# Performance work log

Measured on AMD Instinct MI355X. Metric: run time of the kernel, lower is better.

The kernel has to match this reference:

```python
import jax, jax.numpy as jnp
import numpy as np

DIM = 768
NUM_HEADS = 8
HEAD_DIM = DIM // NUM_HEADS


def setup_inputs() -> dict:
    key = jax.random.key(0)
    k1, k2, k3, k4, k5 = jax.random.split(key, 5)
    B, C, H, W = 16, DIM, 32, 32
    x = jax.random.normal(k1, (B, C, H, W), dtype=jnp.float32)
    # Conv2d 1x1 weights expressed as [out_ch, in_ch] matrices
    w_qkv = jax.random.normal(k2, (3 * C, C), dtype=jnp.float32) * (C ** -0.5)
    b_qkv = jax.random.normal(k3, (3 * C,), dtype=jnp.float32) * 0.02
    w_proj = jax.random.normal(k4, (C, C), dtype=jnp.float32) * (C ** -0.5)
    b_proj = jax.random.normal(k5, (C,), dtype=jnp.float32) * 0.02
    return {"x": x, "w_qkv": w_qkv, "b_qkv": b_qkv, "w_proj": w_proj, "b_proj": b_proj}


def reference(x, w_qkv, b_qkv, w_proj, b_proj):
    B, C, H, W = x.shape
    N = H * W
    nh, hd = NUM_HEADS, C // NUM_HEADS
    xf = x.astype(jnp.float32).reshape(B, C, N)  # bcn
    # 1x1 conv == channel matmul
    qkv = jnp.einsum('oc,bcn->bon', w_qkv, xf) + b_qkv[None, :, None]
    qkv = qkv.reshape(B, 3, nh, hd, N)
    q, k, v = qkv[:, 0], qkv[:, 1], qkv[:, 2]  # [B, nh, hd, N]
    s = hd ** -0.25  # scale split between q and k as in the original
    attn = jnp.einsum('bhdn,bhdm->bhnm', q * s, k * s)  # [B, nh, N, N]
    attn = attn - jax.lax.stop_gradient(jnp.max(attn, axis=-1, keepdims=True))
    attn = jnp.clip(attn, -88.0, 88.0)
    attn = jax.nn.softmax(attn, axis=-1)
    # dropout is identity in eval mode
    out = jnp.einsum('bhnm,bhdm->bhdn', attn, v)  # [B, nh, hd, N]
    out = out.reshape(B, C, N)
    out = jnp.einsum('oc,bcn->bon', w_proj, out) + b_proj[None, :, None]
    return out.reshape(B, C, H, W).astype(x.dtype)
```

## Files before the change

kernel.cpp:

```cpp
#include <hip/hip_runtime.h>
#include <stdint.h>

typedef __attribute__((ext_vector_type(4))) float f32x4;
typedef __attribute__((ext_vector_type(16))) float f32x16;
typedef __attribute__((ext_vector_type(8))) short bf16x8;

#define SQKV 0.38372606f

__device__ __forceinline__ unsigned short f2bf(float f) {
  union { float f; unsigned u; } v; v.f = f;
  unsigned r = v.u + 0x7FFFu + ((v.u >> 16) & 1u);
  return (unsigned short)(r >> 16);
}

__device__ __forceinline__ unsigned cvt_pk_bf16(float a, float b) {
  unsigned r;
  asm volatile("v_cvt_pk_bf16_f32 %0, %1, %2" : "=v"(r) : "v"(a), "v"(b));
  return r;
}
__device__ __forceinline__ void permswap(unsigned &a, unsigned &b) {
  asm volatile("v_permlane32_swap_b32 %0, %1" : "+v"(a), "+v"(b));
}

__device__ __forceinline__ void glds16(const unsigned short* g, unsigned short* l) {
  __builtin_amdgcn_global_load_lds(
      (const __attribute__((address_space(1))) void*)g,
      (__attribute__((address_space(3))) void*)l, 16, 0, 0);
}

__global__ __launch_bounds__(256) void k_convert(const float* __restrict__ src,
                                                 unsigned short* __restrict__ dst,
                                                 int n4) {
  int i = blockIdx.x * 256 + threadIdx.x;
  if (i >= n4) return;
  float4 v = reinterpret_cast<const float4*>(src)[i];
  ushort4 o;
  o.x = f2bf(v.x); o.y = f2bf(v.y); o.z = f2bf(v.z); o.w = f2bf(v.w);
  reinterpret_cast<ushort4*>(dst)[i] = o;
}

__global__ __launch_bounds__(256) void k_transpose(const float* __restrict__ x,
                                                   unsigned short* __restrict__ xT) {
  __shared__ float tile[32][33];
  const int t = threadIdx.x;
  const int j = t & 31, i0 = t >> 5;
  const int n0 = blockIdx.x * 32, c0 = blockIdx.y * 32, b = blockIdx.z;
  const float* src = x + ((size_t)b * 768 + c0) * 1024 + n0;
#pragma unroll
  for (int q = 0; q < 4; ++q)
    tile[i0 + q * 8][j] = src[(size_t)(i0 + q * 8) * 1024 + j];
  __syncthreads();
  unsigned short* dst = xT + ((size_t)b * 1024 + n0) * 768 + c0;
#pragma unroll
  for (int q = 0; q < 4; ++q)
    dst[(size_t)(i0 + q * 8) * 768 + j] = f2bf(tile[j][i0 + q * 8]);
}

__global__ __launch_bounds__(256, 4) void k_gemm_qkv(
    const unsigned short* __restrict__ A,
    const unsigned short* __restrict__ Bx,
    const float* __restrict__ bias,
    unsigned short* __restrict__ qT,
    unsigned short* __restrict__ kT,
    unsigned short* __restrict__ vO) {
  __shared__ unsigned short As[128 * 32];
  __shared__ unsigned short Bs[128 * 32];
  const int t = threadIdx.x;
  const int b = blockIdx.y;
  const int tm = blockIdx.x >> 3, tn = blockIdx.x & 7;
  const int lane = t & 63, w = t >> 6, wr = w >> 1, wc = w & 1;

  const int srow = 16 * w + (lane >> 2);
  const int scol = (lane & 3) * 8;
  const unsigned short* aptr0 = A + (size_t)(tm * 128 + srow) * 768 + scol;
  const unsigned short* aptr1 = aptr0 + (size_t)64 * 768;
  const unsigned short* bptr0 = Bx + (size_t)b * 1024 * 768 + (size_t)(tn * 128 + srow) * 768 + scol;
  const unsigned short* bptr1 = bptr0 + (size_t)64 * 768;
  unsigned short* const lA0 = As + 512 * w;
  unsigned short* const lA1 = As + 2048 + 512 * w;
  unsigned short* const lB0 = Bs + 512 * w;
  unsigned short* const lB1 = Bs + 2048 + 512 * w;

  f32x4 acc[4][4];
#pragma unroll
  for (int mi = 0; mi < 4; ++mi)
#pragma unroll
    for (int ni = 0; ni < 4; ++ni) acc[mi][ni] = (f32x4)0.0f;

  const unsigned short* rA[4];
  const unsigned short* rB[4];
#pragma unroll
  for (int mi = 0; mi < 4; ++mi)
    rA[mi] = As + (wr * 64 + mi * 16 + (lane & 15)) * 32 + ((lane >> 4) << 3);
#pragma unroll
  for (int ni = 0; ni < 4; ++ni)
    rB[ni] = Bs + (wc * 64 + ni * 16 + (lane & 15)) * 32 + ((lane >> 4) << 3);

  for (int kt = 0; kt < 24; ++kt) {
    __syncthreads();
    glds16(aptr0, lA0);
    glds16(aptr1, lA1);
    glds16(bptr0, lB0);
    glds16(bptr1, lB1);
    aptr0 += 32; aptr1 += 32; bptr0 += 32; bptr1 += 32;
    __syncthreads();

    bf16x8 af[4], bfr[4];
#pragma unroll
    for (int mi = 0; mi < 4; ++mi) af[mi] = *reinterpret_cast<const bf16x8*>(rA[mi]);
#pragma unroll
    for (int ni = 0; ni < 4; ++ni) bfr[ni] = *reinterpret_cast<const bf16x8*>(rB[ni]);
#pragma unroll
    for (int mi = 0; mi < 4; ++mi)
#pragma unroll
      for (int ni = 0; ni < 4; ++ni)
        acc[mi][ni] = __builtin_amdgcn_mfma_f32_16x16x32_bf16(af[mi], bfr[ni], acc[mi][ni], 0, 0, 0);
  }

#pragma unroll
  for (int mi = 0; mi < 4; ++mi) {
    const int o0 = tm * 128 + wr * 64 + mi * 16 + ((lane >> 4) << 2);
    const float4 bb = *reinterpret_cast<const float4*>(bias + o0);
    const float sc = (o0 < 1536) ? SQKV : 1.0f;
    const int om = o0 % 768;
    const int hh = om / 96;
    const int d0 = om % 96;
    const int region = o0 / 768;
    const size_t bh = (size_t)(b * 8 + hh);
#pragma unroll
    for (int ni = 0; ni < 4; ++ni) {
      const int nn = tn * 128 + wc * 64 + ni * 16 + (lane & 15);
      ushort4 st;
      st.x = f2bf((acc[mi][ni][0] + bb.x) * sc);
      st.y = f2bf((acc[mi][ni][1] + bb.y) * sc);
      st.z = f2bf((acc[mi][ni][2] + bb.z) * sc);
      st.w = f2bf((acc[mi][ni][3] + bb.w) * sc);
      if (region == 0) {
        *reinterpret_cast<ushort4*>(qT + (bh * 1024 + nn) * 96 + d0) = st;
      } else if (region == 1) {
        *reinterpret_cast<ushort4*>(kT + (bh * 1024 + nn) * 96 + d0) = st;
      } else {
        unsigned short* vp = vO + (bh * 96 + d0) * 1024 + nn;
        vp[0] = st.x; vp[1024] = st.y; vp[2048] = st.z; vp[3072] = st.w;
      }
    }
  }
}

__global__ __launch_bounds__(256, 2) void k_attn2(
    const unsigned short* __restrict__ qT,
    const unsigned short* __restrict__ kT,
    const unsigned short* __restrict__ vO,
    unsigned short* __restrict__ attoutT) {
  __shared__ unsigned short Ks[64][104];
  __shared__ unsigned short Vs[96][72];
  __shared__ float redbuf[4][32];

  const int t = threadIdx.x, lane = t & 63, wv = t >> 6;
  const int r31 = lane & 31, h = lane >> 5;
  const int sw = (blockIdx.x & 7) * 128 + (blockIdx.x >> 3);
  const int bh = sw >> 3, qt = sw & 7;
  const int b = bh >> 3, hh = bh & 7;
  const int n0 = qt * 128 + wv * 32;

  bf16x8 Qf[6];
  {
    const unsigned short* qrow = qT + ((size_t)bh * 1024 + n0 + r31) * 96 + h * 8;
#pragma unroll
    for (int ks = 0; ks < 6; ++ks)
      Qf[ks] = *reinterpret_cast<const bf16x8*>(qrow + ks * 16);
  }

  const unsigned short* gptr[6];
  unsigned short* lptr[6];
#pragma unroll
  for (int i = 0; i < 6; ++i) {
    if (i < 3) {
      const int cc = t + i * 256;
      const int row = cc / 12, col = (cc % 12) * 8;
      gptr[i] = kT + ((size_t)bh * 1024 + row) * 96 + col;
      lptr[i] = &Ks[row][col];
    } else {
      const int cv = t + (i - 3) * 256;
      const int d = cv >> 3, col = (cv & 7) * 8;
      gptr[i] = vO + ((size_t)bh * 96 + d) * 1024 + col;
      lptr[i] = &Vs[d][col];
    }
  }
  uint4 rg[6];
#pragma unroll
  for (int i = 0; i < 6; ++i) rg[i] = *reinterpret_cast<const uint4*>(gptr[i]);

  f32x16 oac[3];
#pragma unroll
  for (int dt = 0; dt < 3; ++dt) oac[dt] = (f32x16)0.0f;
  float run_m = -3.0e38f, run_l = 0.0f;

  for (int mt = 0; mt < 16; ++mt) {
    __syncthreads();
#pragma unroll
    for (int i = 0; i < 6; ++i) *reinterpret_cast<uint4*>(lptr[i]) = rg[i];
    __syncthreads();
    if (mt < 15) {
#pragma unroll
      for (int i = 0; i < 6; ++i) {
        gptr[i] += (i < 3) ? 64 * 96 : 64;
        rg[i] = *reinterpret_cast<const uint4*>(gptr[i]);
      }
    }

    f32x16 sa = (f32x16)0.0f, sb = (f32x16)0.0f;
    __builtin_amdgcn_s_setprio(1);
#pragma unroll
    for (int ks = 0; ks < 6; ++ks) {
      const bf16x8 k0 = *reinterpret_cast<const bf16x8*>(&Ks[r31][ks * 16 + h * 8]);
      const bf16x8 k1 = *reinterpret_cast<const bf16x8*>(&Ks[32 + r31][ks * 16 + h * 8]);
      sa = __builtin_amdgcn_mfma_f32_32x32x16_bf16(k0, Qf[ks], sa, 0, 0, 0);
      sb = __builtin_amdgcn_mfma_f32_32x32x16_bf16(k1, Qf[ks], sb, 0, 0, 0);
    }
    __builtin_amdgcn_s_setprio(0);

    float m4a = fmaxf(sa[0], sa[1]), m4b = fmaxf(sa[2], sa[3]);
    float m4c = fmaxf(sb[0], sb[1]), m4d = fmaxf(sb[2], sb[3]);
#pragma unroll
    for (int i = 4; i < 16; i += 4) {
      m4a = fmaxf(m4a, fmaxf(sa[i], sa[i + 1]));
      m4b = fmaxf(m4b, fmaxf(sa[i + 2], sa[i + 3]));
      m4c = fmaxf(m4c, fmaxf(sb[i], sb[i + 1]));
      m4d = fmaxf(m4d, fmaxf(sb[i + 2], sb[i + 3]));
    }
    float tmax = fmaxf(fmaxf(m4a, m4b), fmaxf(m4c, m4d));
    tmax = fmaxf(tmax, __shfl_xor(tmax, 32));

    if (__any(tmax - run_m > 8.0f)) {
      const float nm = fmaxf(run_m, tmax);
      const float alpha = __builtin_amdgcn_exp2f(run_m - nm);
      run_m = nm;
      run_l *= alpha;
      if (lane < 32) redbuf[wv][lane] = alpha;
      f32x4 a4[4];
#pragma unroll
      for (int q = 0; q < 4; ++q)
        a4[q] = *reinterpret_cast<const f32x4*>(&redbuf[wv][q * 8 + h * 4]);
#pragma unroll
      for (int dt = 0; dt < 3; ++dt)
#pragma unroll
        for (int q = 0; q < 4; ++q)
#pragma unroll
          for (int j = 0; j < 4; ++j)
            oac[dt][q * 4 + j] *= a4[q][j];
    }

    float t0 = 0.f, t1 = 0.f, t2 = 0.f, t3 = 0.f;
#pragma unroll
    for (int i = 0; i < 16; i += 4) {
      sa[i]     = __builtin_amdgcn_exp2f(sa[i] - run_m);     t0 += sa[i];
      sa[i + 1] = __builtin_amdgcn_exp2f(sa[i + 1] - run_m); t1 += sa[i + 1];
      sa[i + 2] = __builtin_amdgcn_exp2f(sa[i + 2] - run_m); t2 += sa[i + 2];
      sa[i + 3] = __builtin_amdgcn_exp2f(sa[i + 3] - run_m); t3 += sa[i + 3];
    }
#pragma unroll
    for (int i = 0; i < 16; i += 4) {
      sb[i]     = __builtin_amdgcn_exp2f(sb[i] - run_m);     t0 += sb[i];
      sb[i + 1] = __builtin_amdgcn_exp2f(sb[i + 1] - run_m); t1 += sb[i + 1];
      sb[i + 2] = __builtin_amdgcn_exp2f(sb[i + 2] - run_m); t2 += sb[i + 2];
      sb[i + 3] = __builtin_amdgcn_exp2f(sb[i + 3] - run_m); t3 += sb[i + 3];
    }
    float ts = (t0 + t1) + (t2 + t3);
    ts += __shfl_xor(ts, 32);
    run_l += ts;

    union { bf16x8 v; unsigned u[4]; } pf;
    __builtin_amdgcn_s_setprio(1);
#pragma unroll
    for (int kst = 0; kst < 4; ++kst) {
      const f32x16& s = (kst < 2) ? sa : sb;
      const int base = (kst & 1) * 8;
      unsigned X = cvt_pk_bf16(s[base + 0], s[base + 1]);
      unsigned Y = cvt_pk_bf16(s[base + 2], s[base + 3]);
      unsigned Z = cvt_pk_bf16(s[base + 4], s[base + 5]);
      unsigned W = cvt_pk_bf16(s[base + 6], s[base + 7]);
      permswap(X, Z);
      permswap(Y, W);
      pf.u[0] = X; pf.u[1] = Y; pf.u[2] = Z; pf.u[3] = W;
#pragma unroll
      for (int dt = 0; dt < 3; ++dt) {
        const bf16x8 vf = *reinterpret_cast<const bf16x8*>(&Vs[dt * 32 + r31][kst * 16 + h * 8]);
        oac[dt] = __builtin_amdgcn_mfma_f32_32x32x16_bf16(pf.v, vf, oac[dt], 0, 0, 0);
      }
    }
    __builtin_amdgcn_s_setprio(0);
  }

  if (lane < 32) redbuf[wv][lane] = 1.0f / run_l;
  f32x4 i4[4];
#pragma unroll
  for (int q = 0; q < 4; ++q)
    i4[q] = *reinterpret_cast<const f32x4*>(&redbuf[wv][q * 8 + h * 4]);
  unsigned short* obase = attoutT + ((size_t)b * 1024 + n0) * 768 + hh * 96;
#pragma unroll
  for (int dt = 0; dt < 3; ++dt)
#pragma unroll
    for (int q = 0; q < 4; ++q)
#pragma unroll
      for (int j = 0; j < 4; ++j) {
        const int np = q * 8 + h * 4 + j;
        obase[(size_t)np * 768 + dt * 32 + r31] = f2bf(oac[dt][q * 4 + j] * i4[q][j]);
      }
}

__global__ __launch_bounds__(256, 4) void k_gemm_proj(
    const unsigned short* __restrict__ Aat,
    const unsigned short* __restrict__ Bw,
    const float* __restrict__ bias,
    float* __restrict__ out) {
  __shared__ unsigned short As[128 * 32];
  __shared__ unsigned short Bs[128 * 32];
  const int t = threadIdx.x;
  const int b = blockIdx.y;
  const int tm = blockIdx.x / 6, tn = blockIdx.x % 6;
  const int lane = t & 63, w = t >> 6, wr = w >> 1, wc = w & 1;

  const int srow = 16 * w + (lane >> 2);
  const int scol = (lane & 3) * 8;
  const unsigned short* aptr0 = Aat + (size_t)b * 1024 * 768 + (size_t)(tm * 128 + srow) * 768 + scol;
  const unsigned short* aptr1 = aptr0 + (size_t)64 * 768;
  const unsigned short* bptr0 = Bw + (size_t)(tn * 128 + srow) * 768 + scol;
  const unsigned short* bptr1 = bptr0 + (size_t)64 * 768;
  unsigned short* const lA0 = As + 512 * w;
  unsigned short* const lA1 = As + 2048 + 512 * w;
  unsigned short* const lB0 = Bs + 512 * w;
  unsigned short* const lB1 = Bs + 2048 + 512 * w;

  f32x4 acc[4][4];
#pragma unroll
  for (int mi = 0; mi < 4; ++mi)
#pragma unroll
    for (int ni = 0; ni < 4; ++ni) acc[mi][ni] = (f32x4)0.0f;

  const unsigned short* rA[4];
  const unsigned short* rB[4];
#pragma unroll
  for (int mi = 0; mi < 4; ++mi)
    rA[mi] = As + (wr * 64 + mi * 16 + (lane & 15)) * 32 + ((lane >> 4) << 3);
#pragma unroll
  for (int ni = 0; ni < 4; ++ni)
    rB[ni] = Bs + (wc * 64 + ni * 16 + (lane & 15)) * 32 + ((lane >> 4) << 3);

  for (int kt = 0; kt < 24; ++kt) {
    __syncthreads();
    glds16(aptr0, lA0);
    glds16(aptr1, lA1);
    glds16(bptr0, lB0);
    glds16(bptr1, lB1);
    aptr0 += 32; aptr1 += 32; bptr0 += 32; bptr1 += 32;
    __syncthreads();

    bf16x8 af[4], bfr[4];
#pragma unroll
    for (int mi = 0; mi < 4; ++mi) af[mi] = *reinterpret_cast<const bf16x8*>(rA[mi]);
#pragma unroll
    for (int ni = 0; ni < 4; ++ni) bfr[ni] = *reinterpret_cast<const bf16x8*>(rB[ni]);
#pragma unroll
    for (int mi = 0; mi < 4; ++mi)
#pragma unroll
      for (int ni = 0; ni < 4; ++ni)
        acc[mi][ni] = __builtin_amdgcn_mfma_f32_16x16x32_bf16(af[mi], bfr[ni], acc[mi][ni], 0, 0, 0);
  }

#pragma unroll
  for (int mi = 0; mi < 4; ++mi) {
    const int n0 = tm * 128 + wr * 64 + mi * 16 + ((lane >> 4) << 2);
#pragma unroll
    for (int ni = 0; ni < 4; ++ni) {
      const int o = tn * 128 + wc * 64 + ni * 16 + (lane & 15);
      const float bo = bias[o];
      float4 vv;
      vv.x = acc[mi][ni][0] + bo;
      vv.y = acc[mi][ni][1] + bo;
      vv.z = acc[mi][ni][2] + bo;
      vv.w = acc[mi][ni][3] + bo;
      *reinterpret_cast<float4*>(out + ((size_t)b * 768 + o) * 1024 + n0) = vv;
    }
  }
}

extern "C" void kernel_launch(void* const* d_in, const int* in_sizes, int n_in,
                              void* d_out, int out_size, void* d_ws, size_t ws_size,
                              hipStream_t stream) {
  const float* x = (const float*)d_in[0];
  const float* w_qkv = (const float*)d_in[1];
  const float* b_qkv = (const float*)d_in[2];
  const float* w_proj = (const float*)d_in[3];
  const float* b_proj = (const float*)d_in[4];
  float* out = (float*)d_out;

  unsigned short* ws = (unsigned short*)d_ws;
  unsigned short* wqkv_bf = ws;
  unsigned short* wproj_bf = wqkv_bf + 2304 * 768;
  unsigned short* xT = wproj_bf + 768 * 768;
  unsigned short* qT = xT + (size_t)16 * 1024 * 768;
  unsigned short* kT = qT + (size_t)16 * 8 * 1024 * 96;
  unsigned short* vO = kT + (size_t)16 * 8 * 1024 * 96;
  unsigned short* attoutT = xT;

  k_convert<<<(2304 * 768 / 4 + 255) / 256, 256, 0, stream>>>(w_qkv, wqkv_bf, 2304 * 768 / 4);
  k_convert<<<(768 * 768 / 4 + 255) / 256, 256, 0, stream>>>(w_proj, wproj_bf, 768 * 768 / 4);
  k_transpose<<<dim3(32, 24, 16), 256, 0, stream>>>(x, xT);
  k_gemm_qkv<<<dim3(144, 16), 256, 0, stream>>>(wqkv_bf, xT, b_qkv, qT, kT, vO);
  k_attn2<<<1024, 256, 0, stream>>>(qT, kT, vO, attoutT);
  k_gemm_proj<<<dim3(48, 16), 256, 0, stream>>>(attoutT, wproj_bf, b_proj, out);
}
```

Before: 263.0 us.

## Double-buffer K/V in LDS and widen attention blocks to 512 threads

The attention kernel now uses 8 waves per block covering 256 queries, so each staged K/V tile is reused by twice as many query rows and K/V global reads are halved. K/V LDS tiles are double-buffered, which removes one barrier per iteration and lets the next tile's stores overlap other waves' compute. This doubles LDS use per block and grows the block, which may affect occupancy and barrier wait cost. A trivial multiply-to-shift change in the GEMMs has no effect.

```diff
diff --git a/kernel.cpp b/kernel.cpp
--- a/kernel.cpp
+++ b/kernel.cpp
@@ -71,7 +71,7 @@
   const int lane = t & 63, w = t >> 6, wr = w >> 1, wc = w & 1;
 
   const int srow = 16 * w + (lane >> 2);
-  const int scol = (lane & 3) * 8;
+  const int scol = (lane & 3) << 3;
   const unsigned short* aptr0 = A + (size_t)(tm * 128 + srow) * 768 + scol;
   const unsigned short* aptr1 = aptr0 + (size_t)64 * 768;
   const unsigned short* bptr0 = Bx + (size_t)b * 1024 * 768 + (size_t)(tn * 128 + srow) * 768 + scol;
@@ -147,21 +147,21 @@
   }
 }
 
-__global__ __launch_bounds__(256, 2) void k_attn2(
+__global__ __launch_bounds__(512, 2) void k_attn2(
     const unsigned short* __restrict__ qT,
     const unsigned short* __restrict__ kT,
     const unsigned short* __restrict__ vO,
     unsigned short* __restrict__ attoutT) {
-  __shared__ unsigned short Ks[64][104];
-  __shared__ unsigned short Vs[96][72];
-  __shared__ float redbuf[4][32];
+  __shared__ unsigned short Ks[2][64 * 104];
+  __shared__ unsigned short Vs[2][96 * 72];
+  __shared__ float redbuf[8][32];
 
   const int t = threadIdx.x, lane = t & 63, wv = t >> 6;
   const int r31 = lane & 31, h = lane >> 5;
-  const int sw = (blockIdx.x & 7) * 128 + (blockIdx.x >> 3);
-  const int bh = sw >> 3, qt = sw & 7;
+  const int sw = (blockIdx.x & 7) * 64 + (blockIdx.x >> 3);
+  const int bh = sw >> 2, qt = sw & 3;
   const int b = bh >> 3, hh = bh & 7;
-  const int n0 = qt * 128 + wv * 32;
+  const int n0 = qt * 256 + wv * 32;
 
   bf16x8 Qf[6];
   {
@@ -171,50 +171,58 @@
       Qf[ks] = *reinterpret_cast<const bf16x8*>(qrow + ks * 16);
   }
 
-  const unsigned short* gptr[6];
-  unsigned short* lptr[6];
-#pragma unroll
-  for (int i = 0; i < 6; ++i) {
-    if (i < 3) {
-      const int cc = t + i * 256;
+  const unsigned short* gptr[3];
+  unsigned short* lptr[3];
+  int gstep[3], lstride[3];
+#pragma unroll
+  for (int i = 0; i < 3; ++i) {
+    const int cc = t + i * 512;
+    if (cc < 768) {
       const int row = cc / 12, col = (cc % 12) * 8;
       gptr[i] = kT + ((size_t)bh * 1024 + row) * 96 + col;
-      lptr[i] = &Ks[row][col];
+      lptr[i] = &Ks[0][row * 104 + col];
+      gstep[i] = 64 * 96;
+      lstride[i] = 64 * 104;
     } else {
-      const int cv = t + (i - 3) * 256;
+      const int cv = cc - 768;
       const int d = cv >> 3, col = (cv & 7) * 8;
       gptr[i] = vO + ((size_t)bh * 96 + d) * 1024 + col;
-      lptr[i] = &Vs[d][col];
-    }
-  }
-  uint4 rg[6];
-#pragma unroll
-  for (int i = 0; i < 6; ++i) rg[i] = *reinterpret_cast<const uint4*>(gptr[i]);
+      lptr[i] = &Vs[0][d * 72 + col];
+      gstep[i] = 64;
+      lstride[i] = 96 * 72;
+    }
+  }
+  uint4 rg[3];
+#pragma unroll
+  for (int i = 0; i < 3; ++i) rg[i] = *reinterpret_cast<const uint4*>(gptr[i]);
 
   f32x16 oac[3];
 #pragma unroll
   for (int dt = 0; dt < 3; ++dt) oac[dt] = (f32x16)0.0f;
   float run_m = -3.0e38f, run_l = 0.0f;
 
-  for (int mt = 0; mt < 16; ++mt) {
-    __syncthreads();
-#pragma unroll
-    for (int i = 0; i < 6; ++i) *reinterpret_cast<uint4*>(lptr[i]) = rg[i];
+  int cur = 0;
+  for (int mt = 0; mt < 16; ++mt, cur ^= 1) {
+#pragma unroll
+    for (int i = 0; i < 3; ++i)
+      *reinterpret_cast<uint4*>(lptr[i] + cur * lstride[i]) = rg[i];
     __syncthreads();
     if (mt < 15) {
 #pragma unroll
-      for (int i = 0; i < 6; ++i) {
-        gptr[i] += (i < 3) ? 64 * 96 : 64;
+      for (int i = 0; i < 3; ++i) {
+        gptr[i] += gstep[i];
         rg[i] = *reinterpret_cast<const uint4*>(gptr[i]);
       }
     }
+    const unsigned short* Kb = &Ks[cur][0];
+    const unsigned short* Vb = &Vs[cur][0];
 
     f32x16 sa = (f32x16)0.0f, sb = (f32x16)0.0f;
     __builtin_amdgcn_s_setprio(1);
 #pragma unroll
     for (int ks = 0; ks < 6; ++ks) {
-      const bf16x8 k0 = *reinterpret_cast<const bf16x8*>(&Ks[r31][ks * 16 + h * 8]);
-      const bf16x8 k1 = *reinterpret_cast<const bf16x8*>(&Ks[32 + r31][ks * 16 + h * 8]);
+      const bf16x8 k0 = *reinterpret_cast<const bf16x8*>(Kb + r31 * 104 + ks * 16 + h * 8);
+      const bf16x8 k1 = *reinterpret_cast<const bf16x8*>(Kb + (32 + r31) * 104 + ks * 16 + h * 8);
       sa = __builtin_amdgcn_mfma_f32_32x32x16_bf16(k0, Qf[ks], sa, 0, 0, 0);
       sb = __builtin_amdgcn_mfma_f32_32x32x16_bf16(k1, Qf[ks], sb, 0, 0, 0);
     }
@@ -285,7 +293,8 @@
       pf.u[0] = X; pf.u[1] = Y; pf.u[2] = Z; pf.u[3] = W;
 #pragma unroll
       for (int dt = 0; dt < 3; ++dt) {
-        const bf16x8 vf = *reinterpret_cast<const bf16x8*>(&Vs[dt * 32 + r31][kst * 16 + h * 8]);
+        const bf16x8 vf = *reinterpret_cast<const bf16x8*>(
+            Vb + (dt * 32 + r31) * 72 + kst * 16 + h * 8);
         oac[dt] = __builtin_amdgcn_mfma_f32_32x32x16_bf16(pf.v, vf, oac[dt], 0, 0, 0);
       }
     }
@@ -322,7 +331,7 @@
   const int lane = t & 63, w = t >> 6, wr = w >> 1, wc = w & 1;
 
   const int srow = 16 * w + (lane >> 2);
-  const int scol = (lane & 3) * 8;
+  const int scol = (lane & 3) << 3;
   const unsigned short* aptr0 = Aat + (size_t)b * 1024 * 768 + (size_t)(tm * 128 + srow) * 768 + scol;
   const unsigned short* aptr1 = aptr0 + (size_t)64 * 768;
   const unsigned short* bptr0 = Bw + (size_t)(tn * 128 + srow) * 768 + scol;
@@ -408,6 +417,6 @@
   k_convert<<<(768 * 768 / 4 + 255) / 256, 256, 0, stream>>>(w_proj, wproj_bf, 768 * 768 / 4);
   k_transpose<<<dim3(32, 24, 16), 256, 0, stream>>>(x, xT);
   k_gemm_qkv<<<dim3(144, 16), 256, 0, stream>>>(wqkv_bf, xT, b_qkv, qT, kT, vO);
-  k_attn2<<<1024, 256, 0, stream>>>(qT, kT, vO, attoutT);
+  k_attn2<<<512, 512, 0, stream>>>(qT, kT, vO, attoutT);
   k_gemm_proj<<<dim3(48, 16), 256, 0, stream>>>(attoutT, wproj_bf, b_proj, out);
 }
```

New measurement: 242.7 us. 1.08x faster.
